# Kernel optimization log

Hardware: AMD Instinct MI355X
Metric: run time of the kernel (lower is better)

The kernel has to match this reference:

```python
import jax, jax.numpy as jnp
import numpy as np

IN, OUT, R = 512, 512, 4
H = (IN + OUT) * R + OUT  # 4608, LSTM hidden size


def setup_inputs() -> dict:
    key = jax.random.key(0)
    ks = jax.random.split(key, 8)
    B = 256
    x = jax.random.normal(ks[0], (B, IN), dtype=jnp.float32)
    h0 = jax.random.normal(ks[1], (B, H), dtype=jnp.float32)
    c0 = jax.random.normal(ks[2], (B, H), dtype=jnp.float32)
    s_ih = 1.0 / np.sqrt(H)
    W_ih = jax.random.uniform(ks[3], (4 * H, IN), dtype=jnp.float32, minval=-s_ih, maxval=s_ih)
    W_hh = jax.random.uniform(ks[4], (4 * H, H), dtype=jnp.float32, minval=-s_ih, maxval=s_ih)
    b_ih = jax.random.uniform(ks[5], (4 * H,), dtype=jnp.float32, minval=-s_ih, maxval=s_ih)
    b_hh = jax.random.uniform(ks[6], (4 * H,), dtype=jnp.float32, minval=-s_ih, maxval=s_ih)
    initial_weight = jax.random.normal(ks[7], (1, OUT, IN), dtype=jnp.float32)
    initial_bias = jnp.zeros((1, OUT), dtype=jnp.float32)
    return {"x": x, "h0": h0, "c0": c0, "W_ih": W_ih, "W_hh": W_hh,
            "b_ih": b_ih, "b_hh": b_hh,
            "initial_weight": initial_weight, "initial_bias": initial_bias}


def reference(x, h0, c0, W_ih, W_hh, b_ih, b_hh, initial_weight, initial_bias):
    B = x.shape[0]
    # Batched LSTMCell (the per-sample python loop in the original is
    # mathematically identical to one batched cell).  PyTorch gate order: i,f,g,o.
    gates = x @ W_ih.T + b_ih + h0 @ W_hh.T + b_hh  # [B, 4H]
    i, f, g, o = jnp.split(gates, 4, axis=-1)
    c_new = jax.nn.sigmoid(f) * c0 + jax.nn.sigmoid(i) * jnp.tanh(g)
    h_new = jax.nn.sigmoid(o) * jnp.tanh(c_new)  # [B, H]
    # Low-rank per-sample weight deltas
    dw1 = h_new[:, : OUT * R].reshape(B, OUT, R)
    dw2 = h_new[:, OUT * R: OUT * R + IN * R].reshape(B, R, IN)
    db = h_new[:, OUT * R + IN * R:]  # [B, OUT]
    weight = initial_weight + jnp.einsum('bor,bri->boi', dw1, dw2)  # [B, OUT, IN]
    bias = initial_bias + db  # [B, OUT]
    y = jnp.einsum('bi,boi->bo', x, weight) + bias
    return (y, h_new, c_new)
```

## Files before the change

kernel.cpp:

```cpp
#include <hip/hip_runtime.h>

#define B_DIM 256
#define H_DIM 4608
#define K_X   512
#define K_TOT 5120
#define KT    32
#define NSTEP (K_TOT / KT)
#define LDA   40

typedef __attribute__((ext_vector_type(8))) short  short8;
typedef __attribute__((ext_vector_type(4))) float  floatx4;

static __device__ __forceinline__ unsigned pkbf(float a, float b){
  unsigned ua = (__float_as_uint(a) + 0x8000u) >> 16;
  unsigned ub = (__float_as_uint(b) + 0x8000u) & 0xFFFF0000u;
  return ua | ub;
}

static __device__ __forceinline__ float sigm(float v){
  return 1.0f / (1.0f + __expf(-v));
}
static __device__ __forceinline__ float tanh_fast(float v){
  float ax = fabsf(v);
  float e  = __expf(-2.0f * ax);
  float t  = (1.0f - e) / (1.0f + e);
  return copysignf(t, v);
}

__global__ __launch_bounds__(256, 2) void lstm_gates_kernel(
    const float* __restrict__ x,   const float* __restrict__ h0,
    const float* __restrict__ c0,
    const float* __restrict__ Wih, const float* __restrict__ Whh,
    const float* __restrict__ bih, const float* __restrict__ bhh,
    float* __restrict__ outH, float* __restrict__ outC)
{
  __shared__ __align__(16) unsigned short As[B_DIM * LDA];
  __shared__ __align__(16) unsigned short Bs[64 * LDA];

  const int t   = threadIdx.x;
  const int j0  = blockIdx.x * 16;
  const int w   = t >> 6;
  const int l   = t & 63;
  const int q   = l >> 4;
  const int col = l & 15;
  const int jj  = j0 + col;

  const int arow = t >> 2;
  const int k8   = (t & 3) * 8;
  const int nloc = t >> 2;
  const int gate = nloc >> 4;
  const int jl   = nloc & 15;
  const long wrowg = (long)gate * H_DIM + j0 + jl;

  long offAx[4], offAh[4];
  #pragma unroll
  for (int rep = 0; rep < 4; ++rep){
    int row = rep * 64 + arow;
    offAx[rep] = (long)row * K_X   + k8;
    offAh[rep] = (long)row * H_DIM + k8;
  }
  const long offBx = wrowg * K_X   + k8;
  const long offBh = wrowg * H_DIM + k8;

  floatx4 acc[4][4];
  #pragma unroll
  for (int nt = 0; nt < 4; ++nt){
    float bsum = bih[nt * H_DIM + jj] + bhh[nt * H_DIM + jj];
    floatx4 v = {bsum, bsum, bsum, bsum};
    #pragma unroll
    for (int mt = 0; mt < 4; ++mt) acc[mt][nt] = v;
  }

  floatx4 pa[4][2];
  floatx4 pb[2];

  auto load_tile = [&](int ko){
    if (ko < K_X){
      #pragma unroll
      for (int rep = 0; rep < 4; ++rep){
        const float* p = x + offAx[rep] + ko;
        pa[rep][0] = *(const floatx4*)p;
        pa[rep][1] = *(const floatx4*)(p + 4);
      }
      const float* pB = Wih + offBx + ko;
      pb[0] = *(const floatx4*)pB;
      pb[1] = *(const floatx4*)(pB + 4);
    } else {
      const int kh = ko - K_X;
      #pragma unroll
      for (int rep = 0; rep < 4; ++rep){
        const float* p = h0 + offAh[rep] + kh;
        pa[rep][0] = *(const floatx4*)p;
        pa[rep][1] = *(const floatx4*)(p + 4);
      }
      const float* pB = Whh + offBh + kh;
      pb[0] = *(const floatx4*)pB;
      pb[1] = *(const floatx4*)(pB + 4);
    }
  };

  load_tile(0);

  const int wrow = w * 64;
  const int aoff = (wrow + col) * LDA + q * 8;
  const int boff = col * LDA + q * 8;

  for (int kt = 0; kt < NSTEP; ++kt){
    __syncthreads();
    #pragma unroll
    for (int rep = 0; rep < 4; ++rep){
      uint4 wv;
      wv.x = pkbf(pa[rep][0].x, pa[rep][0].y);
      wv.y = pkbf(pa[rep][0].z, pa[rep][0].w);
      wv.z = pkbf(pa[rep][1].x, pa[rep][1].y);
      wv.w = pkbf(pa[rep][1].z, pa[rep][1].w);
      *(uint4*)&As[(rep * 64 + arow) * LDA + k8] = wv;
    }
    {
      uint4 wv;
      wv.x = pkbf(pb[0].x, pb[0].y);
      wv.y = pkbf(pb[0].z, pb[0].w);
      wv.z = pkbf(pb[1].x, pb[1].y);
      wv.w = pkbf(pb[1].z, pb[1].w);
      *(uint4*)&Bs[nloc * LDA + k8] = wv;
    }
    __syncthreads();

    if (kt + 1 < NSTEP) load_tile((kt + 1) * KT);

    short8 af[4], bf[4];
    #pragma unroll
    for (int mt = 0; mt < 4; ++mt)
      af[mt] = *(const short8*)&As[aoff + mt * 16 * LDA];
    #pragma unroll
    for (int nt = 0; nt < 4; ++nt)
      bf[nt] = *(const short8*)&Bs[boff + nt * 16 * LDA];
    #pragma unroll
    for (int mt = 0; mt < 4; ++mt)
      #pragma unroll
      for (int nt = 0; nt < 4; ++nt)
        acc[mt][nt] = __builtin_amdgcn_mfma_f32_16x16x32_bf16(af[mt], bf[nt], acc[mt][nt], 0, 0, 0);
  }

  #pragma unroll
  for (int mt = 0; mt < 4; ++mt){
    #pragma unroll
    for (int r = 0; r < 4; ++r){
      int brow = wrow + mt * 16 + q * 4 + r;
      float iv = acc[mt][0][r];
      float fv = acc[mt][1][r];
      float gv = acc[mt][2][r];
      float ov = acc[mt][3][r];
      float cp = c0[(long)brow * H_DIM + jj];
      float cn = sigm(fv) * cp + sigm(iv) * tanh_fast(gv);
      float hn = sigm(ov) * tanh_fast(cn);
      outH[(long)brow * H_DIM + jj] = hn;
      outC[(long)brow * H_DIM + jj] = cn;
    }
  }
}

__global__ __launch_bounds__(256) void y_kernel(
    const float* __restrict__ x, const float* __restrict__ hnew,
    const float* __restrict__ W0, const float* __restrict__ b0,
    float* __restrict__ y)
{
  __shared__ float xs[512];
  __shared__ float zs[4];
  const int b = blockIdx.x;
  const int t = threadIdx.x;
  const int w = t >> 6;
  const int l = t & 63;

  const float* xrow = x + (long)b * 512;
  xs[t]       = xrow[t];
  xs[t + 256] = xrow[t + 256];
  __syncthreads();

  const float* hrow = hnew + (long)b * H_DIM;

  {
    const float* d2 = hrow + 2048 + w * 512;
    float p = 0.f;
    #pragma unroll
    for (int j = 0; j < 8; ++j)
      p += d2[l + 64 * j] * xs[l + 64 * j];
    #pragma unroll
    for (int off = 32; off > 0; off >>= 1)
      p += __shfl_down(p, off);
    if (l == 0) zs[w] = p;
  }
  __syncthreads();
  const float z0 = zs[0], z1 = zs[1], z2 = zs[2], z3 = zs[3];

  for (int oo = 0; oo < 128; ++oo){
    int o = w * 128 + oo;
    const float* wr = W0 + (long)o * 512;
    float p = 0.f;
    #pragma unroll
    for (int j = 0; j < 8; ++j)
      p += wr[l + 64 * j] * xs[l + 64 * j];
    #pragma unroll
    for (int off = 32; off > 0; off >>= 1)
      p += __shfl_down(p, off);
    if (l == 0){
      float4 d1 = *(const float4*)&hrow[o * 4];
      float r = p + b0[o] + hrow[4096 + o]
              + d1.x * z0 + d1.y * z1 + d1.z * z2 + d1.w * z3;
      y[(long)b * 512 + o] = r;
    }
  }
}

extern "C" void kernel_launch(void* const* d_in, const int* in_sizes, int n_in,
                              void* d_out, int out_size, void* d_ws, size_t ws_size,
                              hipStream_t stream)
{
  const float* x   = (const float*)d_in[0];
  const float* h0  = (const float*)d_in[1];
  const float* c0  = (const float*)d_in[2];
  const float* Wih = (const float*)d_in[3];
  const float* Whh = (const float*)d_in[4];
  const float* bih = (const float*)d_in[5];
  const float* bhh = (const float*)d_in[6];
  const float* W0  = (const float*)d_in[7];
  const float* b0  = (const float*)d_in[8];

  float* out  = (float*)d_out;
  float* y    = out;
  float* outH = out + 131072;
  float* outC = out + 131072 + 1179648;

  hipLaunchKernelGGL(lstm_gates_kernel, dim3(288), dim3(256), 0, stream,
                     x, h0, c0, Wih, Whh, bih, bhh, outH, outC);
  hipLaunchKernelGGL(y_kernel, dim3(256), dim3(256), 0, stream,
                     x, outH, W0, b0, y);
}
```

Measured before the change: 727.3 us.

## Split-K the LSTM gate GEMM with workspace partials and separate epilogue

The gate GEMM is split along K into 4 (or 2) chunks so 1152 blocks run instead of 288, which fills more of the GPU's compute units. Each block writes fp32 partial sums to a workspace buffer, and a new epilogue kernel adds the partials and the biases, then applies the LSTM activations. The y kernel is also spread over 4 output chunks per batch row to get more blocks. The cost is extra workspace traffic: each partial is 256x18432 floats, about 18.9 MB, written once and read back. The change also needs a workspace large enough, otherwise the old fused kernel is used.

```diff
diff --git a/kernel.cpp b/kernel.cpp
--- a/kernel.cpp
+++ b/kernel.cpp
@@ -2,11 +2,13 @@
 
 #define B_DIM 256
 #define H_DIM 4608
+#define N_TOT 18432
 #define K_X   512
 #define K_TOT 5120
 #define KT    32
 #define NSTEP (K_TOT / KT)
 #define LDA   40
+#define NJB   288
 
 typedef __attribute__((ext_vector_type(8))) short  short8;
 typedef __attribute__((ext_vector_type(4))) float  floatx4;
@@ -16,7 +18,6 @@
   unsigned ub = (__float_as_uint(b) + 0x8000u) & 0xFFFF0000u;
   return ua | ub;
 }
-
 static __device__ __forceinline__ float sigm(float v){
   return 1.0f / (1.0f + __expf(-v));
 }
@@ -27,7 +28,170 @@
   return copysignf(t, v);
 }
 
-__global__ __launch_bounds__(256, 2) void lstm_gates_kernel(
+template<int KS>
+__global__ __launch_bounds__(256, 5) void gates_gemm_partial(
+    const float* __restrict__ x,   const float* __restrict__ h0,
+    const float* __restrict__ Wih, const float* __restrict__ Whh,
+    float* __restrict__ pbuf)
+{
+  constexpr int KC  = K_TOT / KS;
+  constexpr int NIT = KC / KT;
+
+  __shared__ __align__(16) unsigned short As[B_DIM * LDA];
+  __shared__ __align__(16) unsigned short Bs[64 * LDA];
+
+  const int t    = threadIdx.x;
+  const int jb   = blockIdx.x % NJB;
+  const int kc   = blockIdx.x / NJB;
+  const int j0   = jb * 16;
+  const int kbeg = kc * KC;
+  const int w    = t >> 6;
+  const int l    = t & 63;
+  const int q    = l >> 4;
+  const int col  = l & 15;
+  const int jj   = j0 + col;
+
+  const int arow = t >> 2;
+  const int k8   = (t & 3) * 8;
+  const int nloc = t >> 2;
+  const int gate = nloc >> 4;
+  const int jl   = nloc & 15;
+  const long wrowg = (long)gate * H_DIM + j0 + jl;
+
+  long offAx[4], offAh[4];
+  #pragma unroll
+  for (int rep = 0; rep < 4; ++rep){
+    int row = rep * 64 + arow;
+    offAx[rep] = (long)row * K_X   + k8;
+    offAh[rep] = (long)row * H_DIM + k8;
+  }
+  const long offBx = wrowg * K_X   + k8;
+  const long offBh = wrowg * H_DIM + k8;
+
+  floatx4 acc[4][4];
+  #pragma unroll
+  for (int mt = 0; mt < 4; ++mt)
+    #pragma unroll
+    for (int nt = 0; nt < 4; ++nt)
+      acc[mt][nt] = floatx4{0.f, 0.f, 0.f, 0.f};
+
+  floatx4 pa[4][2];
+  floatx4 pb[2];
+
+  auto load_tile = [&](int ko){
+    if (ko < K_X){
+      #pragma unroll
+      for (int rep = 0; rep < 4; ++rep){
+        const float* p = x + offAx[rep] + ko;
+        pa[rep][0] = *(const floatx4*)p;
+        pa[rep][1] = *(const floatx4*)(p + 4);
+      }
+      const float* pB = Wih + offBx + ko;
+      pb[0] = *(const floatx4*)pB;
+      pb[1] = *(const floatx4*)(pB + 4);
+    } else {
+      const int kh = ko - K_X;
+      #pragma unroll
+      for (int rep = 0; rep < 4; ++rep){
+        const float* p = h0 + offAh[rep] + kh;
+        pa[rep][0] = *(const floatx4*)p;
+        pa[rep][1] = *(const floatx4*)(p + 4);
+      }
+      const float* pB = Whh + offBh + kh;
+      pb[0] = *(const floatx4*)pB;
+      pb[1] = *(const floatx4*)(pB + 4);
+    }
+  };
+
+  load_tile(kbeg);
+
+  const int wrow = w * 64;
+  const int aoff = (wrow + col) * LDA + q * 8;
+  const int boff = col * LDA + q * 8;
+
+  for (int kt = 0; kt < NIT; ++kt){
+    __syncthreads();
+    #pragma unroll
+    for (int rep = 0; rep < 4; ++rep){
+      uint4 wv;
+      wv.x = pkbf(pa[rep][0].x, pa[rep][0].y);
+      wv.y = pkbf(pa[rep][0].z, pa[rep][0].w);
+      wv.z = pkbf(pa[rep][1].x, pa[rep][1].y);
+      wv.w = pkbf(pa[rep][1].z, pa[rep][1].w);
+      *(uint4*)&As[(rep * 64 + arow) * LDA + k8] = wv;
+    }
+    {
+      uint4 wv;
+      wv.x = pkbf(pb[0].x, pb[0].y);
+      wv.y = pkbf(pb[0].z, pb[0].w);
+      wv.z = pkbf(pb[1].x, pb[1].y);
+      wv.w = pkbf(pb[1].z, pb[1].w);
+      *(uint4*)&Bs[nloc * LDA + k8] = wv;
+    }
+    __syncthreads();
+
+    if (kt + 1 < NIT) load_tile(kbeg + (kt + 1) * KT);
+
+    short8 af[4], bf[4];
+    #pragma unroll
+    for (int mt = 0; mt < 4; ++mt)
+      af[mt] = *(const short8*)&As[aoff + mt * 16 * LDA];
+    #pragma unroll
+    for (int nt = 0; nt < 4; ++nt)
+      bf[nt] = *(const short8*)&Bs[boff + nt * 16 * LDA];
+    #pragma unroll
+    for (int mt = 0; mt < 4; ++mt)
+      #pragma unroll
+      for (int nt = 0; nt < 4; ++nt)
+        acc[mt][nt] = __builtin_amdgcn_mfma_f32_16x16x32_bf16(af[mt], bf[nt], acc[mt][nt], 0, 0, 0);
+  }
+
+  float* base = pbuf + (size_t)kc * ((size_t)B_DIM * N_TOT);
+  #pragma unroll
+  for (int mt = 0; mt < 4; ++mt){
+    #pragma unroll
+    for (int r = 0; r < 4; ++r){
+      int brow = wrow + mt * 16 + q * 4 + r;
+      float* rp = base + (size_t)brow * N_TOT + jj;
+      #pragma unroll
+      for (int nt = 0; nt < 4; ++nt)
+        rp[nt * H_DIM] = acc[mt][nt][r];
+    }
+  }
+}
+
+__global__ __launch_bounds__(256) void lstm_epilogue(
+    const float* __restrict__ pbuf, int KS,
+    const float* __restrict__ c0,
+    const float* __restrict__ bih, const float* __restrict__ bhh,
+    float* __restrict__ outH, float* __restrict__ outC)
+{
+  const int b    = blockIdx.x >> 1;
+  const int half = blockIdx.x & 1;
+  const int t    = threadIdx.x;
+  const size_t CH = (size_t)B_DIM * N_TOT;
+
+  for (int it = 0; it < 9; ++it){
+    int j = half * 2304 + it * 256 + t;
+    float g4[4];
+    #pragma unroll
+    for (int g = 0; g < 4; ++g)
+      g4[g] = bih[g * H_DIM + j] + bhh[g * H_DIM + j];
+    for (int kc = 0; kc < KS; ++kc){
+      const float* pp = pbuf + (size_t)kc * CH + (size_t)b * N_TOT + j;
+      #pragma unroll
+      for (int g = 0; g < 4; ++g)
+        g4[g] += pp[g * H_DIM];
+    }
+    float cp = c0[(size_t)b * H_DIM + j];
+    float cn = sigm(g4[1]) * cp + sigm(g4[0]) * tanh_fast(g4[2]);
+    float hn = sigm(g4[3]) * tanh_fast(cn);
+    outH[(size_t)b * H_DIM + j] = hn;
+    outC[(size_t)b * H_DIM + j] = cn;
+  }
+}
+
+__global__ __launch_bounds__(256, 2) void lstm_gates_fused(
     const float* __restrict__ x,   const float* __restrict__ h0,
     const float* __restrict__ c0,
     const float* __restrict__ Wih, const float* __restrict__ Whh,
@@ -167,10 +331,11 @@
 {
   __shared__ float xs[512];
   __shared__ float zs[4];
-  const int b = blockIdx.x;
-  const int t = threadIdx.x;
-  const int w = t >> 6;
-  const int l = t & 63;
+  const int b  = blockIdx.x;
+  const int oc = blockIdx.y;
+  const int t  = threadIdx.x;
+  const int w  = t >> 6;
+  const int l  = t & 63;
 
   const float* xrow = x + (long)b * 512;
   xs[t]       = xrow[t];
@@ -193,8 +358,9 @@
   __syncthreads();
   const float z0 = zs[0], z1 = zs[1], z2 = zs[2], z3 = zs[3];
 
-  for (int oo = 0; oo < 128; ++oo){
-    int o = w * 128 + oo;
+  #pragma unroll 4
+  for (int oo = 0; oo < 32; ++oo){
+    int o = oc * 128 + w * 32 + oo;
     const float* wr = W0 + (long)o * 512;
     float p = 0.f;
     #pragma unroll
@@ -231,8 +397,24 @@
   float* outH = out + 131072;
   float* outC = out + 131072 + 1179648;
 
-  hipLaunchKernelGGL(lstm_gates_kernel, dim3(288), dim3(256), 0, stream,
-                     x, h0, c0, Wih, Whh, bih, bhh, outH, outC);
-  hipLaunchKernelGGL(y_kernel, dim3(256), dim3(256), 0, stream,
+  const size_t chunk = (size_t)B_DIM * N_TOT * sizeof(float);
+  float* pbuf = (float*)d_ws;
+
+  if (ws_size >= 4 * chunk){
+    hipLaunchKernelGGL((gates_gemm_partial<4>), dim3(NJB * 4), dim3(256), 0, stream,
+                       x, h0, Wih, Whh, pbuf);
+    hipLaunchKernelGGL(lstm_epilogue, dim3(512), dim3(256), 0, stream,
+                       pbuf, 4, c0, bih, bhh, outH, outC);
+  } else if (ws_size >= 2 * chunk){
+    hipLaunchKernelGGL((gates_gemm_partial<2>), dim3(NJB * 2), dim3(256), 0, stream,
+                       x, h0, Wih, Whh, pbuf);
+    hipLaunchKernelGGL(lstm_epilogue, dim3(512), dim3(256), 0, stream,
+                       pbuf, 2, c0, bih, bhh, outH, outC);
+  } else {
+    hipLaunchKernelGGL(lstm_gates_fused, dim3(NJB), dim3(256), 0, stream,
+                       x, h0, c0, Wih, Whh, bih, bhh, outH, outC);
+  }
+
+  hipLaunchKernelGGL(y_kernel, dim3(256, 4), dim3(256), 0, stream,
                      x, outH, W0, b0, y);
 }
```

After: 947.3 us. 1.3x slower.

## Pre-convert activations to bf16 and drop LDS staging in gates GEMM

Applied to the files above, without the earlier changes.

Adds a prep kernel that converts the concatenated x/h0 activations to a bf16 workspace once and transposes W0. The gates kernel now loads A fragments and fp32 weight rows straight from global memory into MFMA registers with double-buffered prefetch, removing LDS staging and both syncthreads per K step. The y kernel is split into two blocks per sample and reads transposed W0 with coalesced per-thread columns instead of a serial per-output wave reduction. The cost is an extra launch and workspace traffic, and A is re-read from global/L2 by each wave without LDS sharing.

```diff
diff --git a/kernel.cpp b/kernel.cpp
--- a/kernel.cpp
+++ b/kernel.cpp
@@ -2,21 +2,25 @@
 
 #define B_DIM 256
 #define H_DIM 4608
+#define N_TOT 18432
 #define K_X   512
 #define K_TOT 5120
 #define KT    32
 #define NSTEP (K_TOT / KT)
-#define LDA   40
-
-typedef __attribute__((ext_vector_type(8))) short  short8;
-typedef __attribute__((ext_vector_type(4))) float  floatx4;
+#define NJB   288
+
+typedef __attribute__((ext_vector_type(8))) short    short8;
+typedef __attribute__((ext_vector_type(4))) float    floatx4;
+typedef __attribute__((ext_vector_type(4))) unsigned uintx4;
 
 static __device__ __forceinline__ unsigned pkbf(float a, float b){
   unsigned ua = (__float_as_uint(a) + 0x8000u) >> 16;
   unsigned ub = (__float_as_uint(b) + 0x8000u) & 0xFFFF0000u;
   return ua | ub;
 }
-
+static __device__ __forceinline__ unsigned short bf1(float v){
+  return (unsigned short)((__float_as_uint(v) + 0x8000u) >> 16);
+}
 static __device__ __forceinline__ float sigm(float v){
   return 1.0f / (1.0f + __expf(-v));
 }
@@ -27,40 +31,64 @@
   return copysignf(t, v);
 }
 
-__global__ __launch_bounds__(256, 2) void lstm_gates_kernel(
-    const float* __restrict__ x,   const float* __restrict__ h0,
-    const float* __restrict__ c0,
+__global__ __launch_bounds__(256) void prep_kernel(
+    const float* __restrict__ x, const float* __restrict__ h0,
+    const float* __restrict__ W0,
+    unsigned short* __restrict__ Aws, float* __restrict__ W0T)
+{
+  const int blk = blockIdx.x;
+  const int t   = threadIdx.x;
+  if (blk < 256){
+    const float* xr = x  + (size_t)blk * K_X;
+    const float* hr = h0 + (size_t)blk * H_DIM;
+    unsigned short* ar = Aws + (size_t)blk * K_TOT;
+    #pragma unroll
+    for (int i = 0; i < 20; ++i){
+      int c = i * 256 + t;
+      float v = (c < K_X) ? xr[c] : hr[c - K_X];
+      ar[c] = bf1(v);
+    }
+  } else {
+    int b2 = blk - 256;
+    #pragma unroll
+    for (int i = 0; i < 16; ++i){
+      int idx  = b2 * 4096 + i * 256 + t;
+      int irow = idx >> 9;
+      int o    = idx & 511;
+      W0T[idx] = W0[o * 512 + irow];
+    }
+  }
+}
+
+__global__ __launch_bounds__(256) void gates_kernel(
+    const unsigned short* __restrict__ A,
     const float* __restrict__ Wih, const float* __restrict__ Whh,
     const float* __restrict__ bih, const float* __restrict__ bhh,
+    const float* __restrict__ c0,
     float* __restrict__ outH, float* __restrict__ outC)
 {
-  __shared__ __align__(16) unsigned short As[B_DIM * LDA];
-  __shared__ __align__(16) unsigned short Bs[64 * LDA];
-
-  const int t   = threadIdx.x;
-  const int j0  = blockIdx.x * 16;
-  const int w   = t >> 6;
-  const int l   = t & 63;
-  const int q   = l >> 4;
-  const int col = l & 15;
-  const int jj  = j0 + col;
-
-  const int arow = t >> 2;
-  const int k8   = (t & 3) * 8;
-  const int nloc = t >> 2;
-  const int gate = nloc >> 4;
-  const int jl   = nloc & 15;
-  const long wrowg = (long)gate * H_DIM + j0 + jl;
-
-  long offAx[4], offAh[4];
-  #pragma unroll
-  for (int rep = 0; rep < 4; ++rep){
-    int row = rep * 64 + arow;
-    offAx[rep] = (long)row * K_X   + k8;
-    offAh[rep] = (long)row * H_DIM + k8;
-  }
-  const long offBx = wrowg * K_X   + k8;
-  const long offBh = wrowg * H_DIM + k8;
+  const int t    = threadIdx.x;
+  const int w    = t >> 6;
+  const int l    = t & 63;
+  const int q    = l >> 4;
+  const int col  = l & 15;
+  const int j0   = blockIdx.x * 16;
+  const int jj   = j0 + col;
+  const int wrow = w * 64;
+
+  const unsigned short* pA[4];
+  #pragma unroll
+  for (int mt = 0; mt < 4; ++mt)
+    pA[mt] = A + (size_t)(wrow + mt * 16 + col) * K_TOT + q * 8;
+
+  const float* pBi[4];
+  const float* pBh[4];
+  #pragma unroll
+  for (int nt = 0; nt < 4; ++nt){
+    size_t r = (size_t)nt * H_DIM + jj;
+    pBi[nt] = Wih + r * K_X   + q * 8;
+    pBh[nt] = Whh + r * H_DIM + q * 8;
+  }
 
   floatx4 acc[4][4];
   #pragma unroll
@@ -71,75 +99,53 @@
     for (int mt = 0; mt < 4; ++mt) acc[mt][nt] = v;
   }
 
-  floatx4 pa[4][2];
-  floatx4 pb[2];
-
-  auto load_tile = [&](int ko){
+  short8  aq[2][4];
+  floatx4 bq[2][8];
+
+  auto lda = [&](int u, int ko){
+    #pragma unroll
+    for (int mt = 0; mt < 4; ++mt)
+      aq[u][mt] = *(const short8*)(pA[mt] + ko);
+  };
+  auto ldb = [&](int u, int ko){
     if (ko < K_X){
       #pragma unroll
-      for (int rep = 0; rep < 4; ++rep){
-        const float* p = x + offAx[rep] + ko;
-        pa[rep][0] = *(const floatx4*)p;
-        pa[rep][1] = *(const floatx4*)(p + 4);
+      for (int nt = 0; nt < 4; ++nt){
+        const float* p = pBi[nt] + ko;
+        bq[u][nt * 2]     = *(const floatx4*)p;
+        bq[u][nt * 2 + 1] = *(const floatx4*)(p + 4);
       }
-      const float* pB = Wih + offBx + ko;
-      pb[0] = *(const floatx4*)pB;
-      pb[1] = *(const floatx4*)(pB + 4);
     } else {
-      const int kh = ko - K_X;
+      int kh = ko - K_X;
       #pragma unroll
-      for (int rep = 0; rep < 4; ++rep){
-        const float* p = h0 + offAh[rep] + kh;
-        pa[rep][0] = *(const floatx4*)p;
-        pa[rep][1] = *(const floatx4*)(p + 4);
+      for (int nt = 0; nt < 4; ++nt){
+        const float* p = pBh[nt] + kh;
+        bq[u][nt * 2]     = *(const floatx4*)p;
+        bq[u][nt * 2 + 1] = *(const floatx4*)(p + 4);
       }
-      const float* pB = Whh + offBh + kh;
-      pb[0] = *(const floatx4*)pB;
-      pb[1] = *(const floatx4*)(pB + 4);
     }
   };
-
-  load_tile(0);
-
-  const int wrow = w * 64;
-  const int aoff = (wrow + col) * LDA + q * 8;
-  const int boff = col * LDA + q * 8;
-
-  for (int kt = 0; kt < NSTEP; ++kt){
-    __syncthreads();
-    #pragma unroll
-    for (int rep = 0; rep < 4; ++rep){
-      uint4 wv;
-      wv.x = pkbf(pa[rep][0].x, pa[rep][0].y);
-      wv.y = pkbf(pa[rep][0].z, pa[rep][0].w);
-      wv.z = pkbf(pa[rep][1].x, pa[rep][1].y);
-      wv.w = pkbf(pa[rep][1].z, pa[rep][1].w);
-      *(uint4*)&As[(rep * 64 + arow) * LDA + k8] = wv;
-    }
-    {
-      uint4 wv;
-      wv.x = pkbf(pb[0].x, pb[0].y);
-      wv.y = pkbf(pb[0].z, pb[0].w);
-      wv.z = pkbf(pb[1].x, pb[1].y);
-      wv.w = pkbf(pb[1].z, pb[1].w);
-      *(uint4*)&Bs[nloc * LDA + k8] = wv;
-    }
-    __syncthreads();
-
-    if (kt + 1 < NSTEP) load_tile((kt + 1) * KT);
-
-    short8 af[4], bf[4];
-    #pragma unroll
-    for (int mt = 0; mt < 4; ++mt)
-      af[mt] = *(const short8*)&As[aoff + mt * 16 * LDA];
-    #pragma unroll
-    for (int nt = 0; nt < 4; ++nt)
-      bf[nt] = *(const short8*)&Bs[boff + nt * 16 * LDA];
-    #pragma unroll
-    for (int mt = 0; mt < 4; ++mt)
+  auto comp = [&](int u){
+    #pragma unroll
+    for (int nt = 0; nt < 4; ++nt){
+      floatx4 c0v = bq[u][nt * 2], c1v = bq[u][nt * 2 + 1];
+      uintx4 cv = { pkbf(c0v.x, c0v.y), pkbf(c0v.z, c0v.w),
+                    pkbf(c1v.x, c1v.y), pkbf(c1v.z, c1v.w) };
+      short8 bf = __builtin_bit_cast(short8, cv);
       #pragma unroll
-      for (int nt = 0; nt < 4; ++nt)
-        acc[mt][nt] = __builtin_amdgcn_mfma_f32_16x16x32_bf16(af[mt], bf[nt], acc[mt][nt], 0, 0, 0);
+      for (int mt = 0; mt < 4; ++mt)
+        acc[mt][nt] = __builtin_amdgcn_mfma_f32_16x16x32_bf16(aq[u][mt], bf, acc[mt][nt], 0, 0, 0);
+    }
+  };
+
+  lda(0, 0); ldb(0, 0);
+  for (int kt = 0; kt < NSTEP; kt += 2){
+    int ko1 = (kt + 1) * KT;
+    int ko2 = (kt + 2) * KT;
+    if (ko1 < K_TOT){ lda(1, ko1); ldb(1, ko1); }
+    comp(0);
+    if (ko2 < K_TOT){ lda(0, ko2); ldb(0, ko2); }
+    comp(1);
   }
 
   #pragma unroll
@@ -151,33 +157,35 @@
       float fv = acc[mt][1][r];
       float gv = acc[mt][2][r];
       float ov = acc[mt][3][r];
-      float cp = c0[(long)brow * H_DIM + jj];
+      float cp = c0[(size_t)brow * H_DIM + jj];
       float cn = sigm(fv) * cp + sigm(iv) * tanh_fast(gv);
       float hn = sigm(ov) * tanh_fast(cn);
-      outH[(long)brow * H_DIM + jj] = hn;
-      outC[(long)brow * H_DIM + jj] = cn;
+      outH[(size_t)brow * H_DIM + jj] = hn;
+      outC[(size_t)brow * H_DIM + jj] = cn;
     }
   }
 }
 
 __global__ __launch_bounds__(256) void y_kernel(
     const float* __restrict__ x, const float* __restrict__ hnew,
-    const float* __restrict__ W0, const float* __restrict__ b0,
+    const float* __restrict__ W0T, const float* __restrict__ b0,
     float* __restrict__ y)
 {
   __shared__ float xs[512];
   __shared__ float zs[4];
-  const int b = blockIdx.x;
-  const int t = threadIdx.x;
-  const int w = t >> 6;
-  const int l = t & 63;
-
-  const float* xrow = x + (long)b * 512;
+  const int blk  = blockIdx.x;
+  const int b    = blk >> 1;
+  const int half = blk & 1;
+  const int t    = threadIdx.x;
+  const int w    = t >> 6;
+  const int l    = t & 63;
+
+  const float* xrow = x + (size_t)b * 512;
   xs[t]       = xrow[t];
   xs[t + 256] = xrow[t + 256];
   __syncthreads();
 
-  const float* hrow = hnew + (long)b * H_DIM;
+  const float* hrow = hnew + (size_t)b * H_DIM;
 
   {
     const float* d2 = hrow + 2048 + w * 512;
@@ -191,25 +199,19 @@
     if (l == 0) zs[w] = p;
   }
   __syncthreads();
-  const float z0 = zs[0], z1 = zs[1], z2 = zs[2], z3 = zs[3];
-
-  for (int oo = 0; oo < 128; ++oo){
-    int o = w * 128 + oo;
-    const float* wr = W0 + (long)o * 512;
-    float p = 0.f;
-    #pragma unroll
-    for (int j = 0; j < 8; ++j)
-      p += wr[l + 64 * j] * xs[l + 64 * j];
-    #pragma unroll
-    for (int off = 32; off > 0; off >>= 1)
-      p += __shfl_down(p, off);
-    if (l == 0){
-      float4 d1 = *(const float4*)&hrow[o * 4];
-      float r = p + b0[o] + hrow[4096 + o]
-              + d1.x * z0 + d1.y * z1 + d1.z * z2 + d1.w * z3;
-      y[(long)b * 512 + o] = r;
-    }
-  }
+
+  const int o = half * 256 + t;
+  float p0 = 0.f, p1 = 0.f, p2 = 0.f, p3 = 0.f;
+  for (int k = 0; k < 512; k += 4){
+    p0 += W0T[(size_t)(k + 0) * 512 + o] * xs[k + 0];
+    p1 += W0T[(size_t)(k + 1) * 512 + o] * xs[k + 1];
+    p2 += W0T[(size_t)(k + 2) * 512 + o] * xs[k + 2];
+    p3 += W0T[(size_t)(k + 3) * 512 + o] * xs[k + 3];
+  }
+  float pt = (p0 + p1) + (p2 + p3);
+  float4 d1 = *(const float4*)&hrow[o * 4];
+  y[(size_t)b * 512 + o] = pt + b0[o] + hrow[4096 + o]
+      + d1.x * zs[0] + d1.y * zs[1] + d1.z * zs[2] + d1.w * zs[3];
 }
 
 extern "C" void kernel_launch(void* const* d_in, const int* in_sizes, int n_in,
@@ -231,8 +233,13 @@
   float* outH = out + 131072;
   float* outC = out + 131072 + 1179648;
 
-  hipLaunchKernelGGL(lstm_gates_kernel, dim3(288), dim3(256), 0, stream,
-                     x, h0, c0, Wih, Whh, bih, bhh, outH, outC);
-  hipLaunchKernelGGL(y_kernel, dim3(256), dim3(256), 0, stream,
-                     x, outH, W0, b0, y);
-}
+  unsigned short* Aws = (unsigned short*)d_ws;
+  float* W0T = (float*)((char*)d_ws + (size_t)B_DIM * K_TOT * 2);
+
+  hipLaunchKernelGGL(prep_kernel, dim3(320), dim3(256), 0, stream,
+                     x, h0, W0, Aws, W0T);
+  hipLaunchKernelGGL(gates_kernel, dim3(NJB), dim3(256), 0, stream,
+                     Aws, Wih, Whh, bih, bhh, c0, outH, outC);
+  hipLaunchKernelGGL(y_kernel, dim3(512), dim3(256), 0, stream,
+                     x, outH, W0T, b0, y);
+}
```

New measurement: 876.9 us. +20.6%, slower.
